# Kernel optimization log

Measured on AMD Instinct MI355X. Metric: run time of the kernel, lower is better.

## Reference

```python
import jax, jax.numpy as jnp
import numpy as np

B, BOUNDS, NRIM, K, UNITS = 4096, 512, 6, 4, 600
H_IN, DK_IN, DV_IN = 4, 64, 400
H_C, DK_C, DV_C = 4, 32, 100


def setup_inputs() -> dict:
    key = jax.random.key(0)
    ks = jax.random.split(key, 16)
    s = 0.02
    return {
        'inputs': jax.random.normal(ks[0], (B, BOUNDS + NRIM), jnp.float32),
        'hs': jax.random.normal(ks[1], (B, NRIM, UNITS), jnp.float32) * s,
        'cs': jax.random.normal(ks[2], (B, NRIM, UNITS), jnp.float32) * s,
        'Wk': jax.random.normal(ks[3], (BOUNDS, H_IN * DK_IN), jnp.float32) * s,
        'bk': jnp.zeros((H_IN * DK_IN,), jnp.float32),
        'Wv': jax.random.normal(ks[4], (BOUNDS, H_IN * DV_IN), jnp.float32) * s,
        'bv': jnp.zeros((H_IN * DV_IN,), jnp.float32),
        'Wq': jax.random.normal(ks[5], (NRIM, UNITS, H_IN * DK_IN), jnp.float32) * s,
        'lstm_k': jax.random.normal(ks[6], (NRIM, DV_IN, 4 * UNITS), jnp.float32) * s,
        'lstm_r': jax.random.normal(ks[7], (NRIM, UNITS, 4 * UNITS), jnp.float32) * s,
        'lstm_b': jnp.zeros((NRIM, 4 * UNITS), jnp.float32),
        'Wkc': jax.random.normal(ks[8], (NRIM, UNITS, H_C * DK_C), jnp.float32) * s,
        'Wvc': jax.random.normal(ks[9], (NRIM, UNITS, H_C * DV_C), jnp.float32) * s,
        'Wqc': jax.random.normal(ks[10], (NRIM, UNITS, H_C * DK_C), jnp.float32) * s,
        'Wout': jax.random.normal(ks[11], (NRIM, H_C * DV_C, UNITS), jnp.float32) * s,
    }


def _split_heads(t, n_heads, d_head):
    # [B, T, n_heads*d_head] -> [B, n_heads, T, d_head] (matches tf.split+stack)
    b, t_len = t.shape[0], t.shape[1]
    return t.reshape(b, t_len, n_heads, d_head).transpose(0, 2, 1, 3)


def reference(inputs, hs, cs, Wk, bk, Wv, bv, Wq, lstm_k, lstm_r, lstm_b, Wkc, Wvc, Wqc, Wout):
    x = inputs[:, :BOUNDS]                                   # [B, bounds]
    rim_dist = inputs[:, BOUNDS:BOUNDS + NRIM]               # [B, nRIM]

    # ---- input attention ----
    xx = jnp.stack([x, jnp.zeros_like(x)], axis=1)           # [B, 2, bounds]
    k_lay = xx @ Wk + bk                                     # [B, 2, H*dk]
    v_lay = xx @ Wv + bv                                     # [B, 2, H*dv]
    q_lay = jnp.einsum('bnu,nuo->bno', hs, Wq)               # grouped linear [B, nRIM, H*dq]
    kh = _split_heads(k_lay, H_IN, DK_IN)                    # [B, H, 2, dk]
    vh = _split_heads(v_lay, H_IN, DV_IN)                    # [B, H, 2, dv]
    qh = _split_heads(q_lay, H_IN, DK_IN)                    # [B, H, nRIM, dk]
    v2 = vh.mean(axis=1)                                     # [B, 2, dv]
    scores = jnp.einsum('bhnd,bhtd->bhnt', qh, kh) / np.sqrt(DK_IN).astype(np.float32)
    scores2 = scores.mean(axis=1)                            # [B, nRIM, 2]

    # top-k RIM selection mask from RIM_dist (use_attn=False path)
    _, idx = jax.lax.top_k(rim_dist, K)                      # [B, K]
    mask = jnp.zeros((inputs.shape[0], NRIM), inputs.dtype)
    mask = mask.at[jnp.arange(inputs.shape[0])[:, None], idx].set(1.0)[..., None]  # [B, nRIM, 1]

    probs = jax.nn.softmax(scores2, axis=-1)                 # dropout inactive (training=False)
    rnn_in = jnp.einsum('bnt,btv->bnv', probs, v2) * mask    # [B, nRIM, dv]

    # ---- grouped LSTM (keras gate order i,f,c,o) ----
    gates = (jnp.einsum('bnv,nvo->bno', rnn_in, lstm_k)
             + jnp.einsum('bnu,nuo->bno', hs, lstm_r) + lstm_b)  # [B, nRIM, 4*units]
    i, f, g, o = jnp.split(gates, 4, axis=-1)
    c_rnn = jax.nn.sigmoid(f) * cs + jax.nn.sigmoid(i) * jnp.tanh(g)
    h_rnn = jax.nn.sigmoid(o) * jnp.tanh(c_rnn)
    h_new = jax.lax.stop_gradient(h_rnn * (1.0 - mask)) + h_rnn * mask

    # ---- communication attention among RIMs ----
    kc = _split_heads(jnp.einsum('bnu,nuo->bno', h_new, Wkc), H_C, DK_C)  # [B, Hc, nRIM, dkc]
    vc = _split_heads(jnp.einsum('bnu,nuo->bno', h_new, Wvc), H_C, DV_C)
    qc = _split_heads(jnp.einsum('bnu,nuo->bno', h_new, Wqc), H_C, DK_C)
    sc = jnp.einsum('bhnd,bhmd->bhnm', qc, kc) / np.sqrt(DK_C).astype(np.float32)
    pc = jax.nn.softmax(sc, axis=-1) * mask[:, None, :, :]   # zero rows of inactive query RIMs
    ctx = jnp.einsum('bhnm,bhmv->bhnv', pc, vc)              # [B, Hc, nRIM, dvc]
    ctx = ctx.transpose(0, 2, 1, 3).reshape(inputs.shape[0], NRIM, H_C * DV_C)
    h_comm = jnp.einsum('bno,nou->bnu', ctx, Wout) + h_new   # grouped output proj + residual

    # ---- masked state update ----
    h_upd = h_comm * mask + hs * (1.0 - mask)
    c_upd = c_rnn * mask + cs * (1.0 - mask)
    out_state = h_upd.reshape(inputs.shape[0], UNITS * NRIM)
    return out_state, h_upd, c_upd
```

## Files before the change

kernel.cpp:

```cpp
#include <hip/hip_runtime.h>

namespace {
typedef unsigned short u16;
typedef __attribute__((ext_vector_type(8))) __bf16 bf16x8;
typedef __attribute__((ext_vector_type(4))) float f32x4;

constexpr long long kB  = 4096;
constexpr long long kOS = kB * 3600;
constexpr size_t kGAs = 4096ull * 1088;
constexpr int kHnS = 3648;

constexpr size_t oWkvT  = 0;
constexpr size_t oWqT   = oWkvT  + 768ull*512*2;
constexpr size_t oWcomT = oWqT   + 6ull*256*640*2;
constexpr size_t oWoutT = oWcomT + 6ull*768*640*2;
constexpr size_t oLstmT = oWoutT + 6ull*640*448*2;
constexpr size_t oBp    = oLstmT + 6ull*2432*1024*2;
constexpr size_t oBkv   = oBp    + 6ull*2432*4;
constexpr size_t oMask  = oBkv   + 768*4;
constexpr size_t oArena = oMask  + 4096ull*6*4;
constexpr size_t oGA    = oArena;
constexpr size_t oKV    = oGA   + 6ull*kGAs*2;
constexpr size_t oXbf   = oKV   + 4096ull*768*2;
constexpr size_t oQlay  = oXbf;
constexpr size_t oCqv   = oArena;
constexpr size_t oCtx   = oCqv  + 4096ull*4608*2;
}

__device__ __forceinline__ u16 f2b(float f) {
  union { float f; unsigned u; } x; x.f = f;
  unsigned r = (x.u + 0x7fffu + ((x.u >> 16) & 1u)) >> 16;
  return (u16)r;
}
__device__ __forceinline__ float b2f(u16 u) {
  union { unsigned u; float f; } x; x.u = ((unsigned)u) << 16;
  return x.f;
}
__device__ __forceinline__ float sigmoidf_(float x) { return 1.f / (1.f + __expf(-x)); }
__device__ __forceinline__ float tanhf_(float x) {
  const float e = __expf(2.f * x);
  return 1.f - 2.f / (e + 1.f);
}

__device__ __forceinline__ void gload16(const void* g, void* l) {
  __builtin_amdgcn_global_load_lds((const __attribute__((address_space(1))) void*)g,
                                   (__attribute__((address_space(3))) void*)l, 16, 0, 0);
}

union FragU4 { uint4 u4; bf16x8 v; };

template<int MODE>
__global__ __launch_bounds__(256, 2) void gemm64(
    const u16* __restrict__ A, int lda, long strideA,
    const u16* __restrict__ Bt, long strideB, int Kpad,
    void* __restrict__ C, int ldc, int strideC,
    const float* __restrict__ bias, int strideBias,
    int N, int nks, int storeBf16, int nx, int swz,
    const float* __restrict__ cs, const float* __restrict__ mask,
    float* __restrict__ c_upd, float* __restrict__ h_upd, u16* __restrict__ hnbf,
    const float* __restrict__ hs_in, float* __restrict__ out_state)
{
  __shared__ __align__(16) u16 lds[2 * 16384];

  const int nwg = gridDim.x;
  const int orig = blockIdx.x;
  int wgid;
  {
    const int q = nwg >> 3, r = nwg & 7;
    const int xcd = orig & 7, bidx = orig >> 3;
    wgid = (xcd < r ? xcd * (q + 1) : r * (q + 1) + (xcd - r) * q) + bidx;
  }
  int mt, rim, xt;
  if (swz == 1) {
    rim = wgid / 608;
    const int rem = wgid % 608;
    if (rem < 320) { mt = rem / 10; xt = rem % 10; }
    else           { const int r2 = rem - 320; mt = r2 / 9; xt = 10 + r2 % 9; }
  } else {
    xt = wgid % nx;
    const int t2 = wgid / nx;
    mt = t2 & 31; rim = t2 >> 5;
  }
  const int m0 = mt * 128, n0 = xt * 128;

  A += (size_t)rim * strideA;
  Bt += (size_t)rim * strideB;
  if (bias) bias += (size_t)rim * strideBias;

  const int t = threadIdx.x;
  const int w = t >> 6, lane = t & 63;
  const int lrow = lane & 15, lk = lane >> 4;
  const int wr = w >> 1, wc = w & 1;

  f32x4 acc[4][4] = {};

  const u16* aS[4]; const u16* bS[4]; int cC[4];
#pragma unroll
  for (int i = 0; i < 4; ++i) {
    const int c = t + i * 256;
    const int row = c >> 3, slot = c & 7;
    cC[i] = c;
    aS[i] = A  + (size_t)(m0 + row) * lda  + ((slot ^ (row & 7)) << 3);
    bS[i] = Bt + (size_t)(n0 + row) * Kpad + ((slot ^ (row & 7)) << 3);
  }
  auto stage = [&](u16* dst) {
#pragma unroll
    for (int i = 0; i < 4; ++i) gload16(aS[i], dst + (size_t)cC[i] * 8);
#pragma unroll
    for (int i = 0; i < 4; ++i) gload16(bS[i], dst + 8192 + (size_t)cC[i] * 8);
#pragma unroll
    for (int i = 0; i < 4; ++i) { aS[i] += 64; bS[i] += 64; }
  };

  stage(lds);
  asm volatile("s_waitcnt vmcnt(0)" ::: "memory");
  __builtin_amdgcn_s_barrier();

  for (int s = 0; s < nks; ++s) {
    const bool more = (s + 1 < nks);
    if (more) stage(lds + ((s + 1) & 1) * 16384);
    __builtin_amdgcn_sched_barrier(0);
    const char* Ab = (const char*)(lds + (s & 1) * 16384);
    const char* Bb = Ab + 16384;
#pragma unroll
    for (int ks = 0; ks < 2; ++ks) {
      FragU4 af[4], bf4[4];
#pragma unroll
      for (int mf = 0; mf < 4; ++mf) {
        const int rr = wr * 64 + mf * 16 + lrow;
        af[mf].u4 = *(const uint4*)(Ab + rr * 128 + ((((ks << 2) | lk) ^ (rr & 7)) << 4));
      }
#pragma unroll
      for (int nf = 0; nf < 4; ++nf) {
        const int rr = wc * 64 + nf * 16 + lrow;
        bf4[nf].u4 = *(const uint4*)(Bb + rr * 128 + ((((ks << 2) | lk) ^ (rr & 7)) << 4));
      }
#pragma unroll
      for (int mf = 0; mf < 4; ++mf)
#pragma unroll
        for (int nf = 0; nf < 4; ++nf)
          acc[mf][nf] = __builtin_amdgcn_mfma_f32_16x16x32_bf16(af[mf].v, bf4[nf].v, acc[mf][nf], 0, 0, 0);
    }
    if (more) {
      asm volatile("s_waitcnt vmcnt(0)" ::: "memory");
      __builtin_amdgcn_s_barrier();
    }
  }

  if (MODE == 0) {
    float* Cf = (float*)C + (size_t)rim * strideC;
    u16*   Cu = (u16*)C + (size_t)rim * strideC;
#pragma unroll
    for (int mf = 0; mf < 4; ++mf)
#pragma unroll
      for (int r2 = 0; r2 < 4; ++r2) {
        const int m = m0 + wr * 64 + mf * 16 + 4 * lk + r2;
#pragma unroll
        for (int nf = 0; nf < 4; ++nf) {
          const int col = n0 + wc * 64 + nf * 16 + lrow;
          if (col < N) {
            float v = acc[mf][nf][r2];
            if (bias) v += bias[col];
            const size_t off = (size_t)m * ldc + col;
            if (storeBf16) Cu[off] = f2b(v); else Cf[off] = v;
          }
        }
      }
  } else if (MODE == 1) {
#pragma unroll
    for (int mf = 0; mf < 4; ++mf)
#pragma unroll
      for (int r2 = 0; r2 < 4; ++r2) {
        const int m = m0 + wr * 64 + mf * 16 + 4 * lk + r2;
        const float mk = mask[(size_t)m * 6 + rim];
#pragma unroll
        for (int nf = 0; nf < 4; ++nf) {
          const int col = n0 + wc * 64 + nf * 16 + lrow;
          if (col < 600) {
            const size_t off = (size_t)m * 3600 + rim * 600 + col;
            const float v = (mk != 0.f) ? (acc[mf][nf][r2] + h_upd[off]) : hs_in[off];
            h_upd[off] = v;
            out_state[off] = v;
          }
        }
      }
  } else {
    const int nb = n0 + wc * 64;
    const int u = ((nb >> 6) << 4) + lrow;
    if (u < 600) {
      const float b_i = bias[nb + lrow];
      const float b_f = bias[nb + 16 + lrow];
      const float b_g = bias[nb + 32 + lrow];
      const float b_o = bias[nb + 48 + lrow];
#pragma unroll
      for (int mf = 0; mf < 4; ++mf)
#pragma unroll
        for (int r2 = 0; r2 < 4; ++r2) {
          const int m = m0 + wr * 64 + mf * 16 + 4 * lk + r2;
          const float iv = acc[mf][0][r2] + b_i;
          const float fv = acc[mf][1][r2] + b_f;
          const float gv = acc[mf][2][r2] + b_g;
          const float ov = acc[mf][3][r2] + b_o;
          const size_t off = (size_t)m * 3600 + rim * 600 + u;
          const float cprev = cs[off];
          const float cv = sigmoidf_(fv) * cprev + sigmoidf_(iv) * tanhf_(gv);
          const float hv = sigmoidf_(ov) * tanhf_(cv);
          const float mk = mask[(size_t)m * 6 + rim];
          c_upd[off] = (mk != 0.f) ? cv : cprev;
          h_upd[off] = hv;
          hnbf[(size_t)m * kHnS + rim * 600 + u] = f2b(hv);
        }
    }
  }
}

__device__ void pack_wt_body(float (*tile)[65], int bx, int by, int rim,
    const float* __restrict__ i1, long s1, const float* __restrict__ i2, long s2,
    int K1, int Ktot, int ldin, int Nreal,
    u16* __restrict__ out, long so, int Kpad, int gateperm, int tid)
{
  i1 += (size_t)rim * s1;
  if (i2) i2 += (size_t)rim * s2;
  u16* o = out + (size_t)rim * so;
  const int n0 = bx * 64, k0 = by * 64;
  const int lane = tid & 63, qq = tid >> 6;
  const int n = n0 + lane;
  int col;
  if (gateperm) {
    const int g = (n >> 4) & 3, u = ((n >> 6) << 4) + (n & 15);
    col = (u < 600) ? g * 600 + u : -1;
  } else {
    col = (n < Nreal) ? n : -1;
  }
#pragma unroll
  for (int i = 0; i < 16; ++i) {
    const int kk = qq + 4 * i;
    const int k = k0 + kk;
    float v = 0.f;
    if (col >= 0) {
      if (k < K1) v = i1[(size_t)k * ldin + col];
      else if (k < Ktot) v = i2[(size_t)(k - K1) * ldin + col];
    }
    tile[kk][lane] = v;
  }
  __syncthreads();
#pragma unroll
  for (int i = 0; i < 16; ++i) {
    const int nn = qq + 4 * i;
    const int k = k0 + lane;
    if (k < Kpad) o[(size_t)(n0 + nn) * Kpad + k] = f2b(tile[lane][nn]);
  }
}

__global__ __launch_bounds__(256) void megapack_w(
    const float* __restrict__ Wk, const float* __restrict__ Wv,
    const float* __restrict__ Wkc, const float* __restrict__ Wqc, const float* __restrict__ Wvc,
    const float* __restrict__ Wq, const float* __restrict__ Wout,
    const float* __restrict__ lstm_k, const float* __restrict__ lstm_r,
    u16* __restrict__ WkvT, u16* __restrict__ WcomT, u16* __restrict__ WqT,
    u16* __restrict__ WoutT, u16* __restrict__ LstmT)
{
  __shared__ float tile[64][65];
  const int id = blockIdx.x, t = threadIdx.x;
  if (id < 3648) {
    const int bx = id % 38, by = (id / 38) % 16, bz = id / 608;
    pack_wt_body(tile, bx, by, bz, lstm_k, 400l*2400, lstm_r, 600l*2400,
                 400, 1000, 2400, 2400, LstmT, 2432l*1024, 1024, 1, t);
  } else if (id < 4068) {
    const int i2 = id - 3648;
    const int bx = i2 % 10, by = (i2 / 10) % 7, bz = i2 / 70;
    pack_wt_body(tile, bx, by, bz, Wout, 400l*600, nullptr, 0,
                 400, 400, 600, 600, WoutT, 640l*448, 448, 0, t);
  } else if (id < 4308) {
    const int i3 = id - 4068;
    const int bx = i3 % 4, by = (i3 / 4) % 10, bz = i3 / 40;
    pack_wt_body(tile, bx, by, bz, Wq, 600l*256, nullptr, 0,
                 600, 600, 256, 256, WqT, 256l*640, 640, 0, t);
  } else if (id < 4500) {
    const int e8 = ((id - 4308) * 256 + t) * 8;
    const int n = e8 >> 9, k0 = e8 & 511;
    u16 st[8];
#pragma unroll
    for (int j = 0; j < 8; ++j) {
      const int k = k0 + j;
      float v = 0.f;
      if (n < 256) v = Wk[(size_t)k * 256 + n];
      else if (n < 656) {
        const float* p = Wv + (size_t)k * 1600 + (n - 256);
        v = 0.25f * (p[0] + p[400] + p[800] + p[1200]);
      }
      st[j] = f2b(v);
    }
    *(uint4*)(WkvT + e8) = *(const uint4*)st;
  } else {
    const long long e8 = ((long long)(id - 4500) * 256 + t) * 8;
    const int rim = (int)(e8 / 491520);
    const int rem = (int)(e8 % 491520);
    const int n = rem / 640, k0 = rem % 640;
    u16 st[8];
#pragma unroll
    for (int j = 0; j < 8; ++j) {
      const int k = k0 + j;
      float v = 0.f;
      if (k < 600) {
        if (n < 128)      v = Wkc[(size_t)rim * 76800 + (size_t)k * 128 + n];
        else if (n < 256) v = Wqc[(size_t)rim * 76800 + (size_t)k * 128 + (n - 128)];
        else if (n < 656) v = Wvc[(size_t)rim * 240000 + (size_t)k * 400 + (n - 256)];
      }
      st[j] = f2b(v);
    }
    *(uint4*)(WcomT + e8) = *(const uint4*)st;
  }
}

__global__ __launch_bounds__(256) void megapack_act(
    const float* __restrict__ inputs, const float* __restrict__ hs,
    const float* __restrict__ lstm_b, const float* __restrict__ bk, const float* __restrict__ bv,
    u16* __restrict__ xbf, u16* __restrict__ gA, float* __restrict__ bp, float* __restrict__ bkv,
    u16* __restrict__ hnbf)
{
  __shared__ float row[3600];
  const int id = blockIdx.x, t = threadIdx.x;
  if (id < 4096) {
    const int b = id;
    for (int i = t; i < 3600; i += 256) row[i] = hs[(size_t)b * 3600 + i];
    __syncthreads();
    for (int c = t; c < 516; c += 256) {
      const int rim = c / 86;
      const int j = (c % 86) * 8;
      u16 v[8];
#pragma unroll
      for (int k = 0; k < 8; ++k) {
        const int col = j + k;
        v[k] = (col < 600) ? f2b(row[rim * 600 + col]) : (u16)0;
      }
      *(uint4*)(gA + (size_t)rim * kGAs + (size_t)b * 1088 + 400 + j) = *(const uint4*)v;
    }
    if (t < 6) {
      u16 z[8] = {0,0,0,0,0,0,0,0};
      *(uint4*)(hnbf + (size_t)b * kHnS + 3600 + t * 8) = *(const uint4*)z;
    }
  } else if (id < 5120) {
    const int e8 = ((id - 4096) * 256 + t) * 8;
    const int b = e8 >> 9, c0 = e8 & 511;
    const float* src = inputs + (size_t)b * 518 + c0;
    u16 st[8];
#pragma unroll
    for (int j = 0; j < 8; ++j) st[j] = f2b(src[j]);
    *(uint4*)(xbf + e8) = *(const uint4*)st;
  } else {
    const int tt = (id - 5120) * 256 + t;
    if (tt < 6 * 2432) {
      const int rim = tt / 2432, p = tt % 2432;
      const int g = (p >> 4) & 3, u = ((p >> 6) << 4) + (p & 15);
      bp[tt] = (u < 600) ? lstm_b[(size_t)rim * 2400 + g * 600 + u] : 0.f;
    }
    if (tt < 768) {
      float v = 0.f;
      if (tt < 256) v = bk[tt];
      else if (tt < 656) { const int j2 = tt - 256; v = 0.25f * (bv[j2] + bv[j2+400] + bv[j2+800] + bv[j2+1200]); }
      bkv[tt] = v;
    }
  }
}

__global__ __launch_bounds__(256) void score_kernel(
    const float* __restrict__ inputs, const u16* __restrict__ qlayb,
    const u16* __restrict__ kvb, const float* __restrict__ bk,
    const float* __restrict__ bkv,
    float* __restrict__ maskout, u16* __restrict__ gA)
{
  const int b = blockIdx.x;
  const int t = threadIdx.x;
  __shared__ float red[4][12];
  __shared__ float sprob[12];
  __shared__ float smask[6];

  const float k0v = b2f(kvb[(size_t)b * 768 + t]);
  const float bkv_ = bk[t];
  float part[12];
#pragma unroll
  for (int n = 0; n < 6; ++n) {
    const float q = b2f(qlayb[(size_t)b * 1536 + n * 256 + t]);
    part[2 * n]     = q * k0v;
    part[2 * n + 1] = q * bkv_;
  }
#pragma unroll
  for (int off = 32; off > 0; off >>= 1)
#pragma unroll
    for (int i = 0; i < 12; ++i)
      part[i] += __shfl_down(part[i], off);
  const int wave = t >> 6, lane = t & 63;
  if (lane == 0)
#pragma unroll
    for (int i = 0; i < 12; ++i) red[wave][i] = part[i];
  __syncthreads();
  if (t < 12) red[0][t] = (red[0][t] + red[1][t] + red[2][t] + red[3][t]) * (1.0f / 32.0f);
  __syncthreads();
  if (t < 6) {
    const float s0 = red[0][2 * t], s1 = red[0][2 * t + 1];
    const float mx = fmaxf(s0, s1);
    const float e0 = __expf(s0 - mx), e1 = __expf(s1 - mx);
    const float inv = 1.f / (e0 + e1);
    sprob[2 * t] = e0 * inv;
    sprob[2 * t + 1] = e1 * inv;
    const float* rd = inputs + (size_t)b * 518 + 512;
    const float mine = rd[t];
    int rank = 0;
#pragma unroll
    for (int j = 0; j < 6; ++j) {
      const float o = rd[j];
      rank += (o > mine) || (o == mine && j < t);
    }
    const float mk = (rank < 4) ? 1.f : 0.f;
    smask[t] = mk;
    maskout[(size_t)b * 6 + t] = mk;
  }
  __syncthreads();
  for (int c = t; c < 300; c += 256) {
    const int n = c / 50;
    const int v = (c % 50) * 8;
    const float p0 = sprob[2 * n], p1 = sprob[2 * n + 1], mk = smask[n];
    u16 st[8];
#pragma unroll
    for (int k = 0; k < 8; ++k)
      st[k] = f2b((p0 * b2f(kvb[(size_t)b * 768 + 256 + v + k]) + p1 * bkv[256 + v + k]) * mk);
    *reinterpret_cast<uint4*>(gA + (size_t)n * kGAs + (size_t)b * 1088 + v) =
        *reinterpret_cast<const uint4*>(st);
  }
}

__global__ __launch_bounds__(256) void comm_kernel(
    const u16* __restrict__ cqv, u16* __restrict__ ctx)
{
  const int b = blockIdx.x, t = threadIdx.x;
  __shared__ float skc[768], sqc[768], svc[2400];
  __shared__ float spc[4][6][6];
  for (int i = t * 4; i < 4608; i += 1024) {
    const ushort4 u4 = *reinterpret_cast<const ushort4*>(cqv + (size_t)b * 4608 + i);
    const u16 uu[4] = {u4.x, u4.y, u4.z, u4.w};
#pragma unroll
    for (int j = 0; j < 4; ++j) {
      const int ii = i + j;
      const int m = ii / 768, c = ii % 768;
      const float v = b2f(uu[j]);
      if (c < 128) skc[m * 128 + c] = v;
      else if (c < 256) sqc[m * 128 + (c - 128)] = v;
      else if (c < 656) svc[m * 400 + (c - 256)] = v;
    }
  }
  __syncthreads();
  if (t < 144) {
    const int h = t / 36, n = (t % 36) / 6, m = t % 6;
    float s = 0.f;
#pragma unroll
    for (int d = 0; d < 32; ++d) s += sqc[n * 128 + h * 32 + d] * skc[m * 128 + h * 32 + d];
    spc[h][n][m] = s * 0.17677669529663687f;
  }
  __syncthreads();
  if (t < 24) {
    const int h = t / 6, n = t % 6;
    float mx = -3.0e38f;
#pragma unroll
    for (int m = 0; m < 6; ++m) mx = fmaxf(mx, spc[h][n][m]);
    float e[6], sum = 0.f;
#pragma unroll
    for (int m = 0; m < 6; ++m) { e[m] = __expf(spc[h][n][m] - mx); sum += e[m]; }
    const float inv = 1.f / sum;
#pragma unroll
    for (int m = 0; m < 6; ++m) spc[h][n][m] = e[m] * inv;
  }
  __syncthreads();
  for (int base = t * 4; base < 2400; base += 1024) {
    const int n = base / 400, rr = base % 400, h = rr / 100, v = rr % 100;
    ushort4 st;
    float s0 = 0.f, s1 = 0.f, s2 = 0.f, s3 = 0.f;
#pragma unroll
    for (int m = 0; m < 6; ++m) {
      const float p = spc[h][n][m];
      const float* vm = &svc[m * 400 + h * 100 + v];
      s0 += p * vm[0]; s1 += p * vm[1]; s2 += p * vm[2]; s3 += p * vm[3];
    }
    st.x = f2b(s0); st.y = f2b(s1); st.z = f2b(s2); st.w = f2b(s3);
    *reinterpret_cast<ushort4*>(ctx + (size_t)b * 2400 + base) = st;
  }
}

extern "C" void kernel_launch(void* const* d_in, const int* in_sizes, int n_in,
                              void* d_out, int out_size, void* d_ws, size_t ws_size,
                              hipStream_t stream) {
  const float* inputs = (const float*)d_in[0];
  const float* hs     = (const float*)d_in[1];
  const float* cs     = (const float*)d_in[2];
  const float* Wk     = (const float*)d_in[3];
  const float* bk     = (const float*)d_in[4];
  const float* Wv     = (const float*)d_in[5];
  const float* bv     = (const float*)d_in[6];
  const float* Wq     = (const float*)d_in[7];
  const float* lstm_k = (const float*)d_in[8];
  const float* lstm_r = (const float*)d_in[9];
  const float* lstm_b = (const float*)d_in[10];
  const float* Wkc    = (const float*)d_in[11];
  const float* Wvc    = (const float*)d_in[12];
  const float* Wqc    = (const float*)d_in[13];
  const float* Wout   = (const float*)d_in[14];

  float* out = (float*)d_out;
  float* out_state = out;
  float* h_upd = out + kOS;
  float* c_upd = out + 2 * kOS;
  u16*   hnbf  = (u16*)d_out;

  char* wsb = (char*)d_ws;
  u16* WkvT  = (u16*)(wsb + oWkvT);
  u16* WqT   = (u16*)(wsb + oWqT);
  u16* WcomT = (u16*)(wsb + oWcomT);
  u16* WoutT = (u16*)(wsb + oWoutT);
  u16* LstmT = (u16*)(wsb + oLstmT);
  float* bp    = (float*)(wsb + oBp);
  float* bkv   = (float*)(wsb + oBkv);
  float* maskf = (float*)(wsb + oMask);
  u16* gA    = (u16*)(wsb + oGA);
  u16* kvb   = (u16*)(wsb + oKV);
  u16* xbf   = (u16*)(wsb + oXbf);
  u16* qlayb = (u16*)(wsb + oQlay);
  u16* cqvb  = (u16*)(wsb + oCqv);
  u16* ctxb  = (u16*)(wsb + oCtx);

  dim3 B256(256);

  megapack_w<<<5940, B256, 0, stream>>>(Wk, Wv, Wkc, Wqc, Wvc, Wq, Wout, lstm_k, lstm_r,
                                        WkvT, WcomT, WqT, WoutT, LstmT);
  megapack_act<<<5177, B256, 0, stream>>>(inputs, hs, lstm_b, bk, bv, xbf, gA, bp, bkv, hnbf);

  gemm64<0><<<dim3(192), B256, 0, stream>>>(xbf, 512, 0, WkvT, 0, 512,
      kvb, 768, 0, bkv, 0, 656, 8, 1, 6, 0,
      nullptr, nullptr, nullptr, nullptr, nullptr, nullptr, nullptr);
  gemm64<0><<<dim3(384), B256, 0, stream>>>(gA + 400, 1088, (long)kGAs, WqT, 256l*640, 640,
      qlayb, 1536, 256, nullptr, 0, 256, 10, 1, 2, 0,
      nullptr, nullptr, nullptr, nullptr, nullptr, nullptr, nullptr);

  score_kernel<<<4096, B256, 0, stream>>>(inputs, qlayb, kvb, bk, bkv, maskf, gA);

  gemm64<2><<<dim3(3648), B256, 0, stream>>>(gA, 1088, (long)kGAs, LstmT, 2432l*1024, 1024,
      nullptr, 0, 0, bp, 2432, 2432, 16, 0, 0, 1,
      cs, maskf, c_upd, h_upd, hnbf, nullptr, nullptr);

  gemm64<0><<<dim3(1152), B256, 0, stream>>>(hnbf, kHnS, 600, WcomT, 768l*640, 640,
      cqvb, 4608, 768, nullptr, 0, 656, 10, 1, 6, 0,
      nullptr, nullptr, nullptr, nullptr, nullptr, nullptr, nullptr);

  comm_kernel<<<4096, B256, 0, stream>>>(cqvb, ctxb);

  gemm64<1><<<dim3(960), B256, 0, stream>>>(ctxb, 2400, 400, WoutT, 640l*448, 448,
      nullptr, 0, 0, nullptr, 0, 600, 7, 0, 5, 0,
      nullptr, maskf, nullptr, h_upd, nullptr, hs, out_state);
}
```

Before: 583.8 us.

## Move LSTM gate GEMM to dedicated 256x256-tile kernel with 512 threads

Replaces the 128x128-tile gemm64 MODE 2 path for the LSTM gate GEMM with a new gates256 kernel using 256x256 tiles, 8 waves and a larger double-buffered LDS. The packed LSTM weight N dimension is padded from 2432 to 2560 so it tiles evenly, and the weight and bias packers and workspace offsets change to match. Larger tiles raise arithmetic intensity and cut redundant global loads of A and B. In exchange it adds padded wasted columns, more registers per thread and a smaller grid (960 blocks), which may lower occupancy.

```diff
diff --git a/kernel.cpp b/kernel.cpp
--- a/kernel.cpp
+++ b/kernel.cpp
@@ -15,8 +15,8 @@
 constexpr size_t oWcomT = oWqT   + 6ull*256*640*2;
 constexpr size_t oWoutT = oWcomT + 6ull*768*640*2;
 constexpr size_t oLstmT = oWoutT + 6ull*640*448*2;
-constexpr size_t oBp    = oLstmT + 6ull*2432*1024*2;
-constexpr size_t oBkv   = oBp    + 6ull*2432*4;
+constexpr size_t oBp    = oLstmT + 6ull*2560*1024*2;
+constexpr size_t oBkv   = oBp    + 6ull*2560*4;
 constexpr size_t oMask  = oBkv   + 768*4;
 constexpr size_t oArena = oMask  + 4096ull*6*4;
 constexpr size_t oGA    = oArena;
@@ -55,9 +55,8 @@
     const u16* __restrict__ Bt, long strideB, int Kpad,
     void* __restrict__ C, int ldc, int strideC,
     const float* __restrict__ bias, int strideBias,
-    int N, int nks, int storeBf16, int nx, int swz,
-    const float* __restrict__ cs, const float* __restrict__ mask,
-    float* __restrict__ c_upd, float* __restrict__ h_upd, u16* __restrict__ hnbf,
+    int N, int nks, int storeBf16, int nx,
+    const float* __restrict__ mask, float* __restrict__ h_upd,
     const float* __restrict__ hs_in, float* __restrict__ out_state)
 {
   __shared__ __align__(16) u16 lds[2 * 16384];
@@ -70,17 +69,10 @@
     const int xcd = orig & 7, bidx = orig >> 3;
     wgid = (xcd < r ? xcd * (q + 1) : r * (q + 1) + (xcd - r) * q) + bidx;
   }
-  int mt, rim, xt;
-  if (swz == 1) {
-    rim = wgid / 608;
-    const int rem = wgid % 608;
-    if (rem < 320) { mt = rem / 10; xt = rem % 10; }
-    else           { const int r2 = rem - 320; mt = r2 / 9; xt = 10 + r2 % 9; }
-  } else {
-    xt = wgid % nx;
-    const int t2 = wgid / nx;
-    mt = t2 & 31; rim = t2 >> 5;
-  }
+  const int xt = wgid % nx;
+  const int t2 = wgid / nx;
+  const int mt = t2 & 31;
+  const int rim = t2 >> 5;
   const int m0 = mt * 128, n0 = xt * 128;
 
   A += (size_t)rim * strideA;
@@ -166,7 +158,7 @@
           }
         }
       }
-  } else if (MODE == 1) {
+  } else {
 #pragma unroll
     for (int mf = 0; mf < 4; ++mf)
 #pragma unroll
@@ -184,33 +176,117 @@
           }
         }
       }
-  } else {
-    const int nb = n0 + wc * 64;
-    const int u = ((nb >> 6) << 4) + lrow;
-    if (u < 600) {
-      const float b_i = bias[nb + lrow];
-      const float b_f = bias[nb + 16 + lrow];
-      const float b_g = bias[nb + 32 + lrow];
-      const float b_o = bias[nb + 48 + lrow];
-#pragma unroll
-      for (int mf = 0; mf < 4; ++mf)
-#pragma unroll
-        for (int r2 = 0; r2 < 4; ++r2) {
-          const int m = m0 + wr * 64 + mf * 16 + 4 * lk + r2;
-          const float iv = acc[mf][0][r2] + b_i;
-          const float fv = acc[mf][1][r2] + b_f;
-          const float gv = acc[mf][2][r2] + b_g;
-          const float ov = acc[mf][3][r2] + b_o;
-          const size_t off = (size_t)m * 3600 + rim * 600 + u;
-          const float cprev = cs[off];
-          const float cv = sigmoidf_(fv) * cprev + sigmoidf_(iv) * tanhf_(gv);
-          const float hv = sigmoidf_(ov) * tanhf_(cv);
-          const float mk = mask[(size_t)m * 6 + rim];
-          c_upd[off] = (mk != 0.f) ? cv : cprev;
-          h_upd[off] = hv;
-          hnbf[(size_t)m * kHnS + rim * 600 + u] = f2b(hv);
-        }
-    }
+  }
+}
+
+__global__ __launch_bounds__(512, 2) void gates256(
+    const u16* __restrict__ A, const u16* __restrict__ Bt,
+    const float* __restrict__ bp, const float* __restrict__ cs,
+    const float* __restrict__ mask,
+    float* __restrict__ c_upd, float* __restrict__ h_upd, u16* __restrict__ hnbf)
+{
+  __shared__ __align__(16) u16 lds[2 * 32768];
+
+  const int orig = blockIdx.x;
+  const int wgid = (orig & 7) * 120 + (orig >> 3);
+  const int rim = wgid / 160;
+  const int rem = wgid % 160;
+  const int half = rem / 80;
+  const int r2d = rem % 80;
+  const int mt = r2d / 5;
+  const int xt = half * 5 + r2d % 5;
+  const int m0 = mt * 256, n0 = xt * 256;
+
+  const u16* Ar = A + (size_t)rim * kGAs;
+  const u16* Br = Bt + (size_t)rim * (2560ull * 1024);
+  const float* bip = bp + (size_t)rim * 2560;
+
+  const int t = threadIdx.x;
+  const int w = t >> 6, lane = t & 63;
+  const int lrow = lane & 15, lk = lane >> 4;
+  const int wr = w >> 2, wc = w & 3;
+
+  f32x4 acc[8][4] = {};
+
+  const u16* aS[4]; const u16* bS[4]; int cC[4];
+#pragma unroll
+  for (int i = 0; i < 4; ++i) {
+    const int c = t + i * 512;
+    const int row = c >> 3, slot = c & 7;
+    cC[i] = c;
+    aS[i] = Ar + (size_t)(m0 + row) * 1088 + ((slot ^ (row & 7)) << 3);
+    bS[i] = Br + (size_t)(n0 + row) * 1024 + ((slot ^ (row & 7)) << 3);
+  }
+  auto stage = [&](u16* dst) {
+#pragma unroll
+    for (int i = 0; i < 4; ++i) gload16(aS[i], dst + (size_t)cC[i] * 8);
+#pragma unroll
+    for (int i = 0; i < 4; ++i) gload16(bS[i], dst + 16384 + (size_t)cC[i] * 8);
+#pragma unroll
+    for (int i = 0; i < 4; ++i) { aS[i] += 64; bS[i] += 64; }
+  };
+
+  constexpr int nks = 16;
+  stage(lds);
+  asm volatile("s_waitcnt vmcnt(0)" ::: "memory");
+  __builtin_amdgcn_s_barrier();
+
+  for (int s = 0; s < nks; ++s) {
+    const bool more = (s + 1 < nks);
+    if (more) stage(lds + ((s + 1) & 1) * 32768);
+    __builtin_amdgcn_sched_barrier(0);
+    const char* Ab = (const char*)(lds + (s & 1) * 32768);
+    const char* Bb = Ab + 32768;
+#pragma unroll
+    for (int ks = 0; ks < 2; ++ks) {
+      FragU4 af[8], bf4[4];
+#pragma unroll
+      for (int mf = 0; mf < 8; ++mf) {
+        const int rr = wr * 128 + mf * 16 + lrow;
+        af[mf].u4 = *(const uint4*)(Ab + rr * 128 + ((((ks << 2) | lk) ^ (rr & 7)) << 4));
+      }
+#pragma unroll
+      for (int nf = 0; nf < 4; ++nf) {
+        const int rr = wc * 64 + nf * 16 + lrow;
+        bf4[nf].u4 = *(const uint4*)(Bb + rr * 128 + ((((ks << 2) | lk) ^ (rr & 7)) << 4));
+      }
+#pragma unroll
+      for (int mf = 0; mf < 8; ++mf)
+#pragma unroll
+        for (int nf = 0; nf < 4; ++nf)
+          acc[mf][nf] = __builtin_amdgcn_mfma_f32_16x16x32_bf16(af[mf].v, bf4[nf].v, acc[mf][nf], 0, 0, 0);
+    }
+    if (more) {
+      asm volatile("s_waitcnt vmcnt(0)" ::: "memory");
+      __builtin_amdgcn_s_barrier();
+    }
+  }
+
+  const int nb = n0 + wc * 64;
+  const int u = ((nb >> 6) << 4) + lrow;
+  if (u < 600) {
+    const float b_i = bip[nb + lrow];
+    const float b_f = bip[nb + 16 + lrow];
+    const float b_g = bip[nb + 32 + lrow];
+    const float b_o = bip[nb + 48 + lrow];
+#pragma unroll
+    for (int mf = 0; mf < 8; ++mf)
+#pragma unroll
+      for (int r2 = 0; r2 < 4; ++r2) {
+        const int m = m0 + wr * 128 + mf * 16 + 4 * lk + r2;
+        const float iv = acc[mf][0][r2] + b_i;
+        const float fv = acc[mf][1][r2] + b_f;
+        const float gv = acc[mf][2][r2] + b_g;
+        const float ov = acc[mf][3][r2] + b_o;
+        const size_t off = (size_t)m * 3600 + rim * 600 + u;
+        const float cprev = cs[off];
+        const float cv = sigmoidf_(fv) * cprev + sigmoidf_(iv) * tanhf_(gv);
+        const float hv = sigmoidf_(ov) * tanhf_(cv);
+        const float mk = mask[(size_t)m * 6 + rim];
+        c_upd[off] = (mk != 0.f) ? cv : cprev;
+        h_upd[off] = hv;
+        hnbf[(size_t)m * kHnS + rim * 600 + u] = f2b(hv);
+      }
   }
 }
 
@@ -262,22 +338,22 @@
 {
   __shared__ float tile[64][65];
   const int id = blockIdx.x, t = threadIdx.x;
-  if (id < 3648) {
-    const int bx = id % 38, by = (id / 38) % 16, bz = id / 608;
+  if (id < 3840) {
+    const int bx = id % 40, by = (id / 40) % 16, bz = id / 640;
     pack_wt_body(tile, bx, by, bz, lstm_k, 400l*2400, lstm_r, 600l*2400,
-                 400, 1000, 2400, 2400, LstmT, 2432l*1024, 1024, 1, t);
-  } else if (id < 4068) {
-    const int i2 = id - 3648;
+                 400, 1000, 2400, 2400, LstmT, 2560l*1024, 1024, 1, t);
+  } else if (id < 4260) {
+    const int i2 = id - 3840;
     const int bx = i2 % 10, by = (i2 / 10) % 7, bz = i2 / 70;
     pack_wt_body(tile, bx, by, bz, Wout, 400l*600, nullptr, 0,
                  400, 400, 600, 600, WoutT, 640l*448, 448, 0, t);
-  } else if (id < 4308) {
-    const int i3 = id - 4068;
+  } else if (id < 4500) {
+    const int i3 = id - 4260;
     const int bx = i3 % 4, by = (i3 / 4) % 10, bz = i3 / 40;
     pack_wt_body(tile, bx, by, bz, Wq, 600l*256, nullptr, 0,
                  600, 600, 256, 256, WqT, 256l*640, 640, 0, t);
-  } else if (id < 4500) {
-    const int e8 = ((id - 4308) * 256 + t) * 8;
+  } else if (id < 4692) {
+    const int e8 = ((id - 4500) * 256 + t) * 8;
     const int n = e8 >> 9, k0 = e8 & 511;
     u16 st[8];
 #pragma unroll
@@ -293,7 +369,7 @@
     }
     *(uint4*)(WkvT + e8) = *(const uint4*)st;
   } else {
-    const long long e8 = ((long long)(id - 4500) * 256 + t) * 8;
+    const long long e8 = ((long long)(id - 4692) * 256 + t) * 8;
     const int rim = (int)(e8 / 491520);
     const int rem = (int)(e8 % 491520);
     const int n = rem / 640, k0 = rem % 640;
@@ -350,8 +426,8 @@
     *(uint4*)(xbf + e8) = *(const uint4*)st;
   } else {
     const int tt = (id - 5120) * 256 + t;
-    if (tt < 6 * 2432) {
-      const int rim = tt / 2432, p = tt % 2432;
+    if (tt < 6 * 2560) {
+      const int rim = tt / 2560, p = tt % 2560;
       const int g = (p >> 4) & 3, u = ((p >> 6) << 4) + (p & 15);
       bp[tt] = (u < 600) ? lstm_b[(size_t)rim * 2400 + g * 600 + u] : 0.f;
     }
@@ -529,30 +605,28 @@
 
   dim3 B256(256);
 
-  megapack_w<<<5940, B256, 0, stream>>>(Wk, Wv, Wkc, Wqc, Wvc, Wq, Wout, lstm_k, lstm_r,
+  megapack_w<<<6132, B256, 0, stream>>>(Wk, Wv, Wkc, Wqc, Wvc, Wq, Wout, lstm_k, lstm_r,
                                         WkvT, WcomT, WqT, WoutT, LstmT);
-  megapack_act<<<5177, B256, 0, stream>>>(inputs, hs, lstm_b, bk, bv, xbf, gA, bp, bkv, hnbf);
+  megapack_act<<<5180, B256, 0, stream>>>(inputs, hs, lstm_b, bk, bv, xbf, gA, bp, bkv, hnbf);
 
   gemm64<0><<<dim3(192), B256, 0, stream>>>(xbf, 512, 0, WkvT, 0, 512,
-      kvb, 768, 0, bkv, 0, 656, 8, 1, 6, 0,
-      nullptr, nullptr, nullptr, nullptr, nullptr, nullptr, nullptr);
+      kvb, 768, 0, bkv, 0, 656, 8, 1, 6,
+      nullptr, nullptr, nullptr, nullptr);
   gemm64<0><<<dim3(384), B256, 0, stream>>>(gA + 400, 1088, (long)kGAs, WqT, 256l*640, 640,
-      qlayb, 1536, 256, nullptr, 0, 256, 10, 1, 2, 0,
-      nullptr, nullptr, nullptr, nullptr, nullptr, nullptr, nullptr);
+      qlayb, 1536, 256, nullptr, 0, 256, 10, 1, 2,
+      nullptr, nullptr, nullptr, nullptr);
 
   score_kernel<<<4096, B256, 0, stream>>>(inputs, qlayb, kvb, bk, bkv, maskf, gA);
 
-  gemm64<2><<<dim3(3648), B256, 0, stream>>>(gA, 1088, (long)kGAs, LstmT, 2432l*1024, 1024,
-      nullptr, 0, 0, bp, 2432, 2432, 16, 0, 0, 1,
-      cs, maskf, c_upd, h_upd, hnbf, nullptr, nullptr);
+  gates256<<<dim3(960), dim3(512), 0, stream>>>(gA, LstmT, bp, cs, maskf, c_upd, h_upd, hnbf);
 
   gemm64<0><<<dim3(1152), B256, 0, stream>>>(hnbf, kHnS, 600, WcomT, 768l*640, 640,
-      cqvb, 4608, 768, nullptr, 0, 656, 10, 1, 6, 0,
-      nullptr, nullptr, nullptr, nullptr, nullptr, nullptr, nullptr);
+      cqvb, 4608, 768, nullptr, 0, 656, 10, 1, 6,
+      nullptr, nullptr, nullptr, nullptr);
 
   comm_kernel<<<4096, B256, 0, stream>>>(cqvb, ctxb);
 
   gemm64<1><<<dim3(960), B256, 0, stream>>>(ctxb, 2400, 400, WoutT, 640l*448, 448,
-      nullptr, 0, 0, nullptr, 0, 600, 7, 0, 5, 0,
-      nullptr, maskf, nullptr, h_upd, nullptr, hs, out_state);
-}
+      nullptr, 0, 0, nullptr, 0, 600, 7, 0, 5,
+      maskf, h_upd, hs, out_state);
+}
```

Result: no change. 576.2 us (-1.3%).
